# Kernel tuning notes

Hardware: AMD Instinct MI355X
Metric: run time of the kernel (lower is better)

The kernel has to match this reference:

```python
import jax, jax.numpy as jnp
import numpy as np

EPS_NORM = 1e-12  # F.normalize eps

def _weight_norm(v, g):
    # torch weight_norm with dim=0: W[o,:] = g[o] * v[o,:] / ||v[o,:]||
    return g[:, None] * v / jnp.linalg.norm(v, axis=1, keepdims=True)

def _l2_normalize(x, axis):
    n = jnp.linalg.norm(x, axis=axis, keepdims=True)
    return x / jnp.maximum(n, EPS_NORM)

def setup_inputs() -> dict:
    key = jax.random.key(0)
    ks = jax.random.split(key, 6)
    B, C_emb, T = 16, 1024, 2048
    K, C_cb = 4096, 64
    return {
        "x": jax.random.normal(ks[0], (B, C_emb, T), dtype=jnp.float32),
        "v_in": jax.random.normal(ks[1], (C_cb, C_emb), dtype=jnp.float32) * 0.02,
        "g_in": jax.random.uniform(ks[2], (C_cb,), dtype=jnp.float32, minval=0.5, maxval=1.5),
        "v_out": jax.random.normal(ks[3], (C_emb, C_cb), dtype=jnp.float32) * 0.02,
        "g_out": jax.random.uniform(ks[4], (C_emb,), dtype=jnp.float32, minval=0.5, maxval=1.5),
        "codebook": jax.random.normal(ks[5], (K, C_cb), dtype=jnp.float32),
    }

def reference(x, v_in, g_in, v_out, g_out, codebook):
    sg = jax.lax.stop_gradient
    W_in = _weight_norm(v_in, g_in)    # (C_cb, C_emb)
    W_out = _weight_norm(v_out, g_out)  # (C_emb, C_cb)

    # 1x1 conv projection: (B, C_cb, T)
    x_proj = jnp.einsum('oi,bit->bot', W_in, x)

    # normalize=True: cosine-style nearest neighbor
    emb = _l2_normalize(x_proj, axis=1)           # (B, C_cb, T)
    cb_n = _l2_normalize(codebook, axis=1)        # (K, C_cb)

    e = jnp.swapaxes(emb, 1, 2)                   # (B, T, C_cb)
    # squared euclidean distance (monotone with cdist for argmin)
    dot = jnp.einsum('btc,kc->btk', e, cb_n)      # (B, T, K)
    d2 = (jnp.sum(e * e, axis=-1, keepdims=True)
          - 2.0 * dot
          + jnp.sum(cb_n * cb_n, axis=-1))
    codes = jnp.argmin(d2, axis=-1)               # (B, T) int

    # gather from the UN-normalized codebook (matches torch code)
    quantized_e = codebook[codes]                 # (B, T, C_cb)
    q = jnp.swapaxes(quantized_e, 1, 2)           # (B, C_cb, T)

    codebook_loss = jnp.mean((sg(x_proj) - q) ** 2)
    commit_loss = jnp.mean((x_proj - sg(q)) ** 2)

    quantized_proj = x_proj + sg(q - x_proj)      # straight-through
    quantized = jnp.einsum('oc,bct->bot', W_out, quantized_proj)  # (B, C_emb, T)

    return codes, quantized, codebook_loss, commit_loss, x_proj, quantized_proj
```

## Files before the change

### kernel.cpp

```cpp
#include <hip/hip_runtime.h>
#include <math.h>

#define BB 16
#define CE 1024
#define TT 2048
#define KK 4096
#define CC 64

#define O_CODES 0
#define O_QUANT 32768
#define O_CBL   33587200
#define O_CML   33587201
#define O_XPROJ 33587202
#define O_QPROJ 35684354

#define W_WINF  0
#define W_WOUTF 262144
#define W_CBSQ  327680
#define W_LOSS  659456
#define W_BF    659520

typedef __attribute__((ext_vector_type(8))) _Float16 half8;
typedef __attribute__((ext_vector_type(4))) float f32x4;

__global__ __launch_bounds__(64) void prep_kernel(
    const float* __restrict__ v_in, const float* __restrict__ g_in,
    const float* __restrict__ v_out, const float* __restrict__ g_out,
    const float* __restrict__ cb, float* __restrict__ ws) {
  int bid = blockIdx.x, tid = threadIdx.x;
  if (bid == 0 && tid == 0) ws[W_LOSS] = 0.f;
  if (bid < 64) {
    int o = bid;
    float s = 0.f;
    for (int i = tid; i < CE; i += 64) { float v = v_in[o * CE + i]; s += v * v; }
    for (int off = 32; off; off >>= 1) s += __shfl_down(s, off);
    s = __shfl(s, 0);
    float norm = sqrtf(s);
    float g = g_in[o];
    _Float16* wf = (_Float16*)(ws + W_WINF);
    int ot = o >> 4, m = o & 15;
    for (int i = tid; i < CE; i += 64) {
      float w = (g * v_in[o * CE + i]) / norm;
      _Float16 hi = (_Float16)w;
      _Float16 lo = (_Float16)(w - (float)hi);
      int ks = i >> 5, q = (i >> 3) & 3, j = i & 7;
      int lane = q * 16 + m;
      int base = ((ot * 32 + ks) * 64 + lane) * 8 + j;
      wf[base] = hi;
      wf[65536 + base] = lo;
    }
  } else if (bid < 64 + CE) {
    int o = bid - 64;
    int c = tid;
    float v = v_out[o * CC + c];
    float s = v * v;
    for (int off = 32; off; off >>= 1) s += __shfl_down(s, off);
    s = __shfl(s, 0);
    float w = (g_out[o] * v) / sqrtf(s);
    _Float16 hi = (_Float16)w;
    _Float16 lo = (_Float16)(w - (float)hi);
    _Float16* wf = (_Float16*)(ws + W_WOUTF);
    int ot = o >> 4, m = o & 15;
    int ks = c >> 5, q = (c >> 3) & 3, j = c & 7;
    int lane = q * 16 + m;
    int base = ((ot * 2 + ks) * 64 + lane) * 8 + j;
    wf[base] = hi;
    wf[131072 / 2 + base] = lo;
  } else {
    int k = bid - 64 - CE;
    int c = tid;
    float v = cb[k * CC + c];
    float s = v * v;
    for (int off = 32; off; off >>= 1) s += __shfl_down(s, off);
    s = __shfl(s, 0);
    float n = fmaxf(sqrtf(s), 1e-12f);
    float cn = v / n;
    float s2 = cn * cn;
    for (int off = 32; off; off >>= 1) s2 += __shfl_down(s2, off);
    if (tid == 0) ws[W_CBSQ + k] = s2;
    _Float16 hi = (_Float16)cn;
    _Float16 lo = (_Float16)(cn - (float)hi);
    _Float16* bfh = (_Float16*)(ws + W_BF);
    int ntile = k >> 4, ki = c >> 5;
    int lane = ((c >> 3) & 3) * 16 + (k & 15);
    int j = c & 7;
    int idx = (((ntile * 2 + ki) * 64 + lane) << 3) + j;
    bfh[idx] = hi;
    bfh[262144 + idx] = lo;
  }
}

__global__ __launch_bounds__(256, 2) void fused_kernel(
    const float* __restrict__ x, const float* __restrict__ cb,
    const float* __restrict__ ws, float* __restrict__ out,
    float* loss_acc) {
  __shared__ float xls[64][68];
  __shared__ float nrmS[64];
  __shared__ float pbS[4][64];
  __shared__ int   piS[4][64];
  __shared__ int   codeS[64];

  int tid = threadIdx.x;
  int w = tid >> 6, l = tid & 63;
  int n = l & 15, q = l >> 4;
  int blk = blockIdx.x;
  int b = blk >> 5, t0 = (blk & 31) * 64;

  const half8* wfin = (const half8*)(ws + W_WINF);
  const half8* wfo  = (const half8*)(ws + W_WOUTF);
  const half8* bfr  = (const half8*)(ws + W_BF);
  const float* cbsq = ws + W_CBSQ;

  {
    int t = t0 + w * 16 + n;
    const float* xp = x + (size_t)b * CE * TT + t;
    f32x4 acc[4];
#pragma unroll
    for (int ot = 0; ot < 4; ++ot) acc[ot] = (f32x4){0.f, 0.f, 0.f, 0.f};

    float v[2][8];
    half8 wh[2][4], wl[2][4];
#pragma unroll
    for (int j = 0; j < 8; ++j) v[0][j] = xp[(size_t)(q * 8 + j) * TT];
#pragma unroll
    for (int ot = 0; ot < 4; ++ot) {
      wh[0][ot] = wfin[(ot * 32 + 0) * 64 + l];
      wl[0][ot] = wfin[8192 + (ot * 32 + 0) * 64 + l];
    }
#pragma unroll 2
    for (int ks = 0; ks < 32; ++ks) {
      int cur = ks & 1;
      if (ks < 31) {
        int kb = (ks + 1) * 32 + q * 8;
#pragma unroll
        for (int j = 0; j < 8; ++j) v[cur ^ 1][j] = xp[(size_t)(kb + j) * TT];
#pragma unroll
        for (int ot = 0; ot < 4; ++ot) {
          wh[cur ^ 1][ot] = wfin[(ot * 32 + ks + 1) * 64 + l];
          wl[cur ^ 1][ot] = wfin[8192 + (ot * 32 + ks + 1) * 64 + l];
        }
      }
      half8 xh, xl;
#pragma unroll
      for (int j = 0; j < 8; ++j) xh[j] = (_Float16)v[cur][j];
#pragma unroll
      for (int j = 0; j < 8; ++j) xl[j] = (_Float16)(v[cur][j] - (float)xh[j]);
#pragma unroll
      for (int ot = 0; ot < 4; ++ot)
        acc[ot] = __builtin_amdgcn_mfma_f32_16x16x32_f16(wh[cur][ot], xh, acc[ot], 0, 0, 0);
#pragma unroll
      for (int ot = 0; ot < 4; ++ot)
        acc[ot] = __builtin_amdgcn_mfma_f32_16x16x32_f16(wh[cur][ot], xl, acc[ot], 0, 0, 0);
#pragma unroll
      for (int ot = 0; ot < 4; ++ot)
        acc[ot] = __builtin_amdgcn_mfma_f32_16x16x32_f16(wl[cur][ot], xh, acc[ot], 0, 0, 0);
    }

    float s = 0.f;
    int tl = w * 16 + n;
#pragma unroll
    for (int ot = 0; ot < 4; ++ot) {
#pragma unroll
      for (int r = 0; r < 4; ++r) {
        float vv = acc[ot][r];
        out[O_XPROJ + (size_t)(b * CC + ot * 16 + q * 4 + r) * TT + t] = vv;
        s = fmaf(vv, vv, s);
      }
      *(f32x4*)&xls[tl][ot * 16 + q * 4] = acc[ot];
    }
    s += __shfl_xor(s, 16);
    s += __shfl_xor(s, 32);
    if (l < 16) nrmS[tl] = fmaxf(sqrtf(s), 1e-12f);
  }
  __syncthreads();

  {
    half8 Ahi[4][2], Alo[4][2];
#pragma unroll
    for (int bd = 0; bd < 4; ++bd) {
      int tl = bd * 16 + n;
      float nv = nrmS[tl];
#pragma unroll
      for (int ki = 0; ki < 2; ++ki) {
#pragma unroll
        for (int j = 0; j < 8; ++j) {
          float vv = xls[tl][ki * 32 + q * 8 + j] / nv;
          _Float16 h = (_Float16)vv;
          Ahi[bd][ki][j] = h;
          Alo[bd][ki][j] = (_Float16)(vv - (float)h);
        }
      }
    }

    float best[4][4];
    int bidx[4][4];
#pragma unroll
    for (int bd = 0; bd < 4; ++bd)
#pragma unroll
      for (int r = 0; r < 4; ++r) { best[bd][r] = 3.4e38f; bidx[bd][r] = 0; }

    half8 Bh0[2], Bh1[2], Bl0[2], Bl1[2];
    float cq[2];
    {
      int nt = w * 64;
      Bh0[0] = bfr[(nt * 2 + 0) * 64 + l];
      Bh1[0] = bfr[(nt * 2 + 1) * 64 + l];
      Bl0[0] = bfr[32768 + (nt * 2 + 0) * 64 + l];
      Bl1[0] = bfr[32768 + (nt * 2 + 1) * 64 + l];
      cq[0] = cbsq[nt * 16 + n];
    }
#pragma unroll 2
    for (int it = 0; it < 64; ++it) {
      int cur = it & 1;
      int nt = w * 64 + it;
      if (it < 63) {
        int nt2 = nt + 1;
        Bh0[cur ^ 1] = bfr[(nt2 * 2 + 0) * 64 + l];
        Bh1[cur ^ 1] = bfr[(nt2 * 2 + 1) * 64 + l];
        Bl0[cur ^ 1] = bfr[32768 + (nt2 * 2 + 0) * 64 + l];
        Bl1[cur ^ 1] = bfr[32768 + (nt2 * 2 + 1) * 64 + l];
        cq[cur ^ 1] = cbsq[nt2 * 16 + n];
      }
      f32x4 acc[4];
#pragma unroll
      for (int bd = 0; bd < 4; ++bd) acc[bd] = (f32x4){0.f, 0.f, 0.f, 0.f};
#pragma unroll
      for (int bd = 0; bd < 4; ++bd)
        acc[bd] = __builtin_amdgcn_mfma_f32_16x16x32_f16(Ahi[bd][0], Bh0[cur], acc[bd], 0, 0, 0);
#pragma unroll
      for (int bd = 0; bd < 4; ++bd)
        acc[bd] = __builtin_amdgcn_mfma_f32_16x16x32_f16(Ahi[bd][1], Bh1[cur], acc[bd], 0, 0, 0);
#pragma unroll
      for (int bd = 0; bd < 4; ++bd)
        acc[bd] = __builtin_amdgcn_mfma_f32_16x16x32_f16(Alo[bd][0], Bh0[cur], acc[bd], 0, 0, 0);
#pragma unroll
      for (int bd = 0; bd < 4; ++bd)
        acc[bd] = __builtin_amdgcn_mfma_f32_16x16x32_f16(Alo[bd][1], Bh1[cur], acc[bd], 0, 0, 0);
#pragma unroll
      for (int bd = 0; bd < 4; ++bd)
        acc[bd] = __builtin_amdgcn_mfma_f32_16x16x32_f16(Ahi[bd][0], Bl0[cur], acc[bd], 0, 0, 0);
#pragma unroll
      for (int bd = 0; bd < 4; ++bd)
        acc[bd] = __builtin_amdgcn_mfma_f32_16x16x32_f16(Ahi[bd][1], Bl1[cur], acc[bd], 0, 0, 0);

      int kl = nt * 16 + n;
#pragma unroll
      for (int bd = 0; bd < 4; ++bd)
#pragma unroll
        for (int r = 0; r < 4; ++r) {
          float sc = fmaf(-2.f, acc[bd][r], cq[cur]);
          if (sc < best[bd][r]) { best[bd][r] = sc; bidx[bd][r] = kl; }
        }
    }

#pragma unroll
    for (int st = 1; st < 16; st <<= 1) {
#pragma unroll
      for (int bd = 0; bd < 4; ++bd)
#pragma unroll
        for (int r = 0; r < 4; ++r) {
          float os = __shfl_xor(best[bd][r], st);
          int oi = __shfl_xor(bidx[bd][r], st);
          if (os < best[bd][r] || (os == best[bd][r] && oi < bidx[bd][r])) {
            best[bd][r] = os;
            bidx[bd][r] = oi;
          }
        }
    }
    if (n == 0) {
#pragma unroll
      for (int bd = 0; bd < 4; ++bd)
#pragma unroll
        for (int r = 0; r < 4; ++r) {
          int tl = bd * 16 + q * 4 + r;
          pbS[w][tl] = best[bd][r];
          piS[w][tl] = bidx[bd][r];
        }
    }
  }
  __syncthreads();

  if (tid < 64) {
    float bs = pbS[0][tid];
    int bi = piS[0][tid];
#pragma unroll
    for (int s = 1; s < 4; ++s) {
      float s2 = pbS[s][tid];
      int i2 = piS[s][tid];
      if (s2 < bs || (s2 == bs && i2 < bi)) { bs = s2; bi = i2; }
    }
    codeS[tid] = bi;
    out[O_CODES + b * TT + t0 + tid] = (float)bi;
  }
  __syncthreads();

  {
    int t = t0 + w * 16 + n;
    int tl = w * 16 + n;
    int code = codeS[tl];
    const float* cbr = cb + (size_t)code * CC;
    float qv[2][8];
#pragma unroll
    for (int ks = 0; ks < 2; ++ks) {
      float4 a = *(const float4*)&cbr[ks * 32 + q * 8];
      float4 c4 = *(const float4*)&cbr[ks * 32 + q * 8 + 4];
      qv[ks][0] = a.x; qv[ks][1] = a.y; qv[ks][2] = a.z; qv[ks][3] = a.w;
      qv[ks][4] = c4.x; qv[ks][5] = c4.y; qv[ks][6] = c4.z; qv[ks][7] = c4.w;
    }

    float ls = 0.f;
#pragma unroll
    for (int ks = 0; ks < 2; ++ks)
#pragma unroll
      for (int j = 0; j < 8; ++j) {
        int c = ks * 32 + q * 8 + j;
        float qq = qv[ks][j];
        out[O_QPROJ + (size_t)(b * CC + c) * TT + t] = qq;
        float d = xls[tl][c] - qq;
        ls = fmaf(d, d, ls);
      }
    for (int off = 32; off; off >>= 1) ls += __shfl_down(ls, off);
    if (l == 0) atomicAdd(loss_acc, ls);

    half8 qh[2], ql[2];
#pragma unroll
    for (int ks = 0; ks < 2; ++ks)
#pragma unroll
      for (int j = 0; j < 8; ++j) {
        qh[ks][j] = (_Float16)qv[ks][j];
        ql[ks][j] = (_Float16)(qv[ks][j] - (float)qh[ks][j]);
      }

    half8 wc[2][4];
    wc[0][0] = wfo[0 * 64 + l];
    wc[0][1] = wfo[1 * 64 + l];
    wc[0][2] = wfo[8192 + 0 * 64 + l];
    wc[0][3] = wfo[8192 + 1 * 64 + l];
#pragma unroll 2
    for (int ot = 0; ot < 64; ++ot) {
      int cur = ot & 1;
      if (ot < 63) {
        int o2 = ot + 1;
        wc[cur ^ 1][0] = wfo[(o2 * 2 + 0) * 64 + l];
        wc[cur ^ 1][1] = wfo[(o2 * 2 + 1) * 64 + l];
        wc[cur ^ 1][2] = wfo[8192 + (o2 * 2 + 0) * 64 + l];
        wc[cur ^ 1][3] = wfo[8192 + (o2 * 2 + 1) * 64 + l];
      }
      f32x4 acc = (f32x4){0.f, 0.f, 0.f, 0.f};
      acc = __builtin_amdgcn_mfma_f32_16x16x32_f16(wc[cur][0], qh[0], acc, 0, 0, 0);
      acc = __builtin_amdgcn_mfma_f32_16x16x32_f16(wc[cur][1], qh[1], acc, 0, 0, 0);
      acc = __builtin_amdgcn_mfma_f32_16x16x32_f16(wc[cur][0], ql[0], acc, 0, 0, 0);
      acc = __builtin_amdgcn_mfma_f32_16x16x32_f16(wc[cur][1], ql[1], acc, 0, 0, 0);
      acc = __builtin_amdgcn_mfma_f32_16x16x32_f16(wc[cur][2], qh[0], acc, 0, 0, 0);
      acc = __builtin_amdgcn_mfma_f32_16x16x32_f16(wc[cur][3], qh[1], acc, 0, 0, 0);
#pragma unroll
      for (int r = 0; r < 4; ++r)
        out[O_QUANT + (size_t)(b * CE + ot * 16 + q * 4 + r) * TT + t] = acc[r];
    }
  }
}

__global__ void finalize_kernel(const float* __restrict__ ws, float* __restrict__ out) {
  if (threadIdx.x == 0 && blockIdx.x == 0) {
    float l = ws[W_LOSS] / 2097152.f;
    out[O_CBL] = l;
    out[O_CML] = l;
  }
}

extern "C" void kernel_launch(void* const* d_in, const int* in_sizes, int n_in,
                              void* d_out, int out_size, void* d_ws, size_t ws_size,
                              hipStream_t stream) {
  const float* x     = (const float*)d_in[0];
  const float* v_in  = (const float*)d_in[1];
  const float* g_in  = (const float*)d_in[2];
  const float* v_out = (const float*)d_in[3];
  const float* g_out = (const float*)d_in[4];
  const float* cb    = (const float*)d_in[5];
  float* out = (float*)d_out;
  float* ws  = (float*)d_ws;

  prep_kernel<<<64 + 1024 + 4096, 64, 0, stream>>>(v_in, g_in, v_out, g_out, cb, ws);
  fused_kernel<<<512, 256, 0, stream>>>(x, cb, ws, out, ws + W_LOSS);
  finalize_kernel<<<1, 64, 0, stream>>>(ws, out);
}
```

Before: 346.9 us.

## Double fused-kernel block to 8 waves, splitting codebook search and output projection

The fused kernel now launches 512 threads per block instead of 256. Only the first four waves run the input projection. All eight waves split the 4096-entry codebook search in halves of 32 N-tiles each, and the final argmin reduction merges eight partial results instead of four. In the output projection, waves are paired so each covers half of the 1024 output channels, and only one of each pair writes quantized_proj and the loss. The goal is more in-flight waves per CU to hide memory and MFMA latency. The tighter launch bound (512, 4) may force register spills given the large per-thread A fragments.

```diff
diff --git a/kernel.cpp b/kernel.cpp
--- a/kernel.cpp
+++ b/kernel.cpp
@@ -90,14 +90,14 @@
   }
 }
 
-__global__ __launch_bounds__(256, 2) void fused_kernel(
+__global__ __launch_bounds__(512, 4) void fused_kernel(
     const float* __restrict__ x, const float* __restrict__ cb,
     const float* __restrict__ ws, float* __restrict__ out,
     float* loss_acc) {
   __shared__ float xls[64][68];
   __shared__ float nrmS[64];
-  __shared__ float pbS[4][64];
-  __shared__ int   piS[4][64];
+  __shared__ float pbS[8][64];
+  __shared__ int   piS[8][64];
   __shared__ int   codeS[64];
 
   int tid = threadIdx.x;
@@ -111,7 +111,7 @@
   const half8* bfr  = (const half8*)(ws + W_BF);
   const float* cbsq = ws + W_CBSQ;
 
-  {
+  if (w < 4) {
     int t = t0 + w * 16 + n;
     const float* xp = x + (size_t)b * CE * TT + t;
     f32x4 acc[4];
@@ -201,8 +201,9 @@
 
     half8 Bh0[2], Bh1[2], Bl0[2], Bl1[2];
     float cq[2];
+    int ntb = w * 32;
     {
-      int nt = w * 64;
+      int nt = ntb;
       Bh0[0] = bfr[(nt * 2 + 0) * 64 + l];
       Bh1[0] = bfr[(nt * 2 + 1) * 64 + l];
       Bl0[0] = bfr[32768 + (nt * 2 + 0) * 64 + l];
@@ -210,10 +211,10 @@
       cq[0] = cbsq[nt * 16 + n];
     }
 #pragma unroll 2
-    for (int it = 0; it < 64; ++it) {
+    for (int it = 0; it < 32; ++it) {
       int cur = it & 1;
-      int nt = w * 64 + it;
-      if (it < 63) {
+      int nt = ntb + it;
+      if (it < 31) {
         int nt2 = nt + 1;
         Bh0[cur ^ 1] = bfr[(nt2 * 2 + 0) * 64 + l];
         Bh1[cur ^ 1] = bfr[(nt2 * 2 + 1) * 64 + l];
@@ -284,7 +285,7 @@
     float bs = pbS[0][tid];
     int bi = piS[0][tid];
 #pragma unroll
-    for (int s = 1; s < 4; ++s) {
+    for (int s = 1; s < 8; ++s) {
       float s2 = pbS[s][tid];
       int i2 = piS[s][tid];
       if (s2 < bs || (s2 == bs && i2 < bi)) { bs = s2; bi = i2; }
@@ -295,8 +296,9 @@
   __syncthreads();
 
   {
-    int t = t0 + w * 16 + n;
-    int tl = w * 16 + n;
+    int tg = w & 3, oh = w >> 2;
+    int t = t0 + tg * 16 + n;
+    int tl = tg * 16 + n;
     int code = codeS[tl];
     const float* cbr = cb + (size_t)code * CC;
     float qv[2][8];
@@ -308,19 +310,21 @@
       qv[ks][4] = c4.x; qv[ks][5] = c4.y; qv[ks][6] = c4.z; qv[ks][7] = c4.w;
     }
 
-    float ls = 0.f;
-#pragma unroll
-    for (int ks = 0; ks < 2; ++ks)
-#pragma unroll
-      for (int j = 0; j < 8; ++j) {
-        int c = ks * 32 + q * 8 + j;
-        float qq = qv[ks][j];
-        out[O_QPROJ + (size_t)(b * CC + c) * TT + t] = qq;
-        float d = xls[tl][c] - qq;
-        ls = fmaf(d, d, ls);
-      }
-    for (int off = 32; off; off >>= 1) ls += __shfl_down(ls, off);
-    if (l == 0) atomicAdd(loss_acc, ls);
+    if (oh == 0) {
+      float ls = 0.f;
+#pragma unroll
+      for (int ks = 0; ks < 2; ++ks)
+#pragma unroll
+        for (int j = 0; j < 8; ++j) {
+          int c = ks * 32 + q * 8 + j;
+          float qq = qv[ks][j];
+          out[O_QPROJ + (size_t)(b * CC + c) * TT + t] = qq;
+          float d = xls[tl][c] - qq;
+          ls = fmaf(d, d, ls);
+        }
+      for (int off = 32; off; off >>= 1) ls += __shfl_down(ls, off);
+      if (l == 0) atomicAdd(loss_acc, ls);
+    }
 
     half8 qh[2], ql[2];
 #pragma unroll
@@ -331,15 +335,17 @@
         ql[ks][j] = (_Float16)(qv[ks][j] - (float)qh[ks][j]);
       }
 
+    int ob = oh * 32;
     half8 wc[2][4];
-    wc[0][0] = wfo[0 * 64 + l];
-    wc[0][1] = wfo[1 * 64 + l];
-    wc[0][2] = wfo[8192 + 0 * 64 + l];
-    wc[0][3] = wfo[8192 + 1 * 64 + l];
+    wc[0][0] = wfo[(ob * 2 + 0) * 64 + l];
+    wc[0][1] = wfo[(ob * 2 + 1) * 64 + l];
+    wc[0][2] = wfo[8192 + (ob * 2 + 0) * 64 + l];
+    wc[0][3] = wfo[8192 + (ob * 2 + 1) * 64 + l];
 #pragma unroll 2
-    for (int ot = 0; ot < 64; ++ot) {
-      int cur = ot & 1;
-      if (ot < 63) {
+    for (int i = 0; i < 32; ++i) {
+      int cur = i & 1;
+      int ot = ob + i;
+      if (i < 31) {
         int o2 = ot + 1;
         wc[cur ^ 1][0] = wfo[(o2 * 2 + 0) * 64 + l];
         wc[cur ^ 1][1] = wfo[(o2 * 2 + 1) * 64 + l];
@@ -381,6 +387,6 @@
   float* ws  = (float*)d_ws;
 
   prep_kernel<<<64 + 1024 + 4096, 64, 0, stream>>>(v_in, g_in, v_out, g_out, cb, ws);
-  fused_kernel<<<512, 256, 0, stream>>>(x, cb, ws, out, ws + W_LOSS);
+  fused_kernel<<<512, 512, 0, stream>>>(x, cb, ws, out, ws + W_LOSS);
   finalize_kernel<<<1, 64, 0, stream>>>(ws, out);
 }
```

Result: slower. 608.0 us (+75.3%).
